# Kernel tuning notes

Hardware: AMD Instinct MI355X
Metric: run time of the kernel (lower is better)

## Reference

```python
import jax, jax.numpy as jnp
import numpy as np

B, H, W, C = 64, 56, 56, 128
NH, WS, SS = 4, 7, 3        # heads, window_size, shift_size
HID = 4 * C                  # mlp hidden
HD = C // NH                 # head dim
SCALE = HD ** -0.5
NW = (H // WS) * (W // WS)   # windows per image
L = WS * WS                  # tokens per window


def _rel_pos_index():
    coords = np.stack(np.meshgrid(np.arange(WS), np.arange(WS), indexing='ij'))  # (2,WS,WS)
    cf = coords.reshape(2, -1)
    rel = (cf[:, :, None] - cf[:, None, :]).transpose(1, 2, 0)  # (L,L,2)
    rel[:, :, 0] += WS - 1
    rel[:, :, 1] += WS - 1
    rel[:, :, 0] *= 2 * WS - 1
    return rel.sum(-1)  # (L,L) int


def _attn_mask():
    # standard Swin shifted-window mask, computed statically in numpy
    img = np.zeros((H, W), dtype=np.int32)
    cnt = 0
    for hs in (slice(0, -WS), slice(-WS, -SS), slice(-SS, None)):
        for ws_ in (slice(0, -WS), slice(-WS, -SS), slice(-SS, None)):
            img[hs, ws_] = cnt
            cnt += 1
    win = img.reshape(H // WS, WS, W // WS, WS).transpose(0, 2, 1, 3).reshape(NW, L)
    diff = win[:, None, :] - win[:, :, None]
    return np.where(diff != 0, -100.0, 0.0).astype(np.float32)  # (NW,L,L)


_REL_IDX = jnp.asarray(_rel_pos_index())
_MASK = jnp.asarray(_attn_mask())


def _layernorm(x, w, b, eps=1e-5):
    mu = x.mean(-1, keepdims=True)
    var = x.var(-1, keepdims=True)
    return (x - mu) * jax.lax.rsqrt(var + eps) * w + b


def setup_inputs() -> dict:
    key = jax.random.key(0)
    ks = jax.random.split(key, 8)
    n = lambda k, s: jax.random.normal(k, s, jnp.float32) * 0.02
    return {
        'x': jax.random.normal(ks[0], (B, H * W, C), jnp.float32),
        'norm1_w': jnp.ones((C,)), 'norm1_b': jnp.zeros((C,)),
        'qkv_w': n(ks[1], (3 * C, C)), 'qkv_b': jnp.zeros((3 * C,)),
        'proj_w': n(ks[2], (C, C)), 'proj_b': jnp.zeros((C,)),
        'rel_bias': n(ks[3], ((2 * WS - 1) ** 2, NH)),
        'norm2_w': jnp.ones((C,)), 'norm2_b': jnp.zeros((C,)),
        'fc1_w': n(ks[4], (HID, C)), 'fc1_b': jnp.zeros((HID,)),
        'fc2_w': n(ks[5], (C, HID)), 'fc2_b': jnp.zeros((C,)),
    }


def reference(x, norm1_w, norm1_b, qkv_w, qkv_b, proj_w, proj_b, rel_bias,
              norm2_w, norm2_b, fc1_w, fc1_b, fc2_w, fc2_b):
    shortcut = x
    h = _layernorm(x, norm1_w, norm1_b).reshape(B, H, W, C)
    # cyclic shift
    h = jnp.roll(h, shift=(-SS, -SS), axis=(1, 2))
    # window partition -> (B*NW, L, C)
    h = h.reshape(B, H // WS, WS, W // WS, WS, C).transpose(0, 1, 3, 2, 4, 5)
    h = h.reshape(B * NW, L, C)
    # qkv
    qkv = h @ qkv_w.T + qkv_b                      # (B*NW, L, 3C)
    qkv = qkv.reshape(B * NW, L, 3, NH, HD).transpose(2, 0, 3, 1, 4)
    q, k, v = qkv[0], qkv[1], qkv[2]               # (B*NW, NH, L, HD)
    attn = jnp.einsum('wnld,wnmd->wnlm', q * SCALE, k)  # (B*NW, NH, L, L)
    bias = rel_bias[_REL_IDX.reshape(-1)].reshape(L, L, NH).transpose(2, 0, 1)
    attn = attn + bias[None]
    # shifted-window mask
    attn = attn.reshape(B, NW, NH, L, L) + _MASK[None, :, None]
    attn = jax.nn.softmax(attn.reshape(B * NW, NH, L, L), axis=-1)
    out = jnp.einsum('wnlm,wnmd->wnld', attn, v)   # (B*NW, NH, L, HD)
    out = out.transpose(0, 2, 1, 3).reshape(B * NW, L, C)
    out = out @ proj_w.T + proj_b
    # window reverse
    out = out.reshape(B, H // WS, W // WS, WS, WS, C).transpose(0, 1, 3, 2, 4, 5)
    out = out.reshape(B, H, W, C)
    out = jnp.roll(out, shift=(SS, SS), axis=(1, 2)).reshape(B, H * W, C)
    x = shortcut + out
    # MLP
    y = _layernorm(x, norm2_w, norm2_b)
    y = jax.nn.gelu(y @ fc1_w.T + fc1_b, approximate=False)
    x = x + (y @ fc2_w.T + fc2_b)
    return x
```

## Files before the change

kernel.cpp:

```cpp
#include <hip/hip_runtime.h>
#include <math.h>


typedef unsigned int   u32;
typedef unsigned short u16;
typedef __bf16 bf16_t;
typedef __bf16 bf16x8 __attribute__((ext_vector_type(8)));
typedef float  f32x4  __attribute__((ext_vector_type(4)));

#define KSCALE 0.17677669529663687f

__device__ __forceinline__ float lo2f(u32 u){ u32 v = u << 16;         float f; __builtin_memcpy(&f,&v,4); return f; }
__device__ __forceinline__ float hi2f(u32 u){ u32 v = u & 0xffff0000u; float f; __builtin_memcpy(&f,&v,4); return f; }
__device__ __forceinline__ float b2f(u16 h){ u32 v = (u32)h << 16;     float f; __builtin_memcpy(&f,&v,4); return f; }
__device__ __forceinline__ u16  f2b(float f){ bf16_t h = (bf16_t)f; u16 u; __builtin_memcpy(&u,&h,2); return u; }
__device__ __forceinline__ u32  pack2(float a, float b){ return (u32)f2b(a) | ((u32)f2b(b) << 16); }

template<int C>
__device__ __forceinline__ float dppf(float x){
  union { float f; int i; } u; u.f = x;
  u.i = __builtin_amdgcn_update_dpp(u.i, u.i, C, 0xf, 0xf, true);
  return u.f;
}
__device__ __forceinline__ float red16max(float x){
  x = fmaxf(x, dppf<0xB1>(x));
  x = fmaxf(x, dppf<0x4E>(x));
  x = fmaxf(x, dppf<0x141>(x));
  x = fmaxf(x, dppf<0x140>(x));
  return x;
}
__device__ __forceinline__ float red16sum(float x){
  x += dppf<0xB1>(x);
  x += dppf<0x4E>(x);
  x += dppf<0x141>(x);
  x += dppf<0x140>(x);
  return x;
}
__device__ __forceinline__ float red64sum(float x){
  x = red16sum(x);
  x += __shfl_xor(x, 16, 64);
  x += __shfl_xor(x, 32, 64);
  return x;
}

template<bool F32> __device__ __forceinline__ float2 ldpair(const void* p, size_t pairIdx){
  if constexpr (F32) { return ((const float2*)p)[pairIdx]; }
  else { u32 u = ((const u32*)p)[pairIdx]; return float2{lo2f(u), hi2f(u)}; }
}
template<bool F32> __device__ __forceinline__ float ldone(const void* p, size_t i){
  if constexpr (F32) return ((const float*)p)[i];
  else               return b2f(((const u16*)p)[i]);
}
template<bool F32> __device__ __forceinline__ void stpair(void* p, size_t pairIdx, float a, float b){
  if constexpr (F32) ((float2*)p)[pairIdx] = float2{a, b};
  else               ((u32*)p)[pairIdx] = pack2(a, b);
}

__device__ __forceinline__ float gelu_f(float v){
  const float t = v * v;
  const float u = v * (1.5957691216057308f + 0.07135481282803452f * t);
  return v * __builtin_amdgcn_rcpf(1.f + __expf(-u));
}

__device__ __align__(16) u16 g_wbuf[197312];

__global__ __launch_bounds__(256) void k_cvt(const void* n1w, const void* qkvw,
    const void* projw, const void* fc1w, const void* fc2w, const void* relb)
{
  const bool bf = (((const u32*)n1w)[0] == 0x3F803F80u);
  u16* o = g_wbuf;
  if (blockIdx.x == 192) {
    const int t = threadIdx.x;
    if (t < 169) {
      const int i = t * 4;
      if (bf) { *(uint2*)(o + 196608 + i) = *(const uint2*)((const u16*)relb + i); }
      else {
        const float4 v = *(const float4*)((const float*)relb + i);
        uint2 pk; pk.x = pack2(v.x, v.y); pk.y = pack2(v.z, v.w);
        *(uint2*)(o + 196608 + i) = pk;
      }
    } else if (t < 176) {
      *(uint2*)(o + 196608 + 676 + (t - 169) * 4) = uint2{0, 0};
    }
    return;
  }
  const int i = (blockIdx.x * 256 + threadIdx.x) * 4;
  const void* src; int rel; u16* dst;
  if (i < 49152)       { src = qkvw; rel = i;          dst = o; }
  else if (i < 65536)  { src = projw; rel = i - 49152; dst = o + 49152; }
  else if (i < 131072) { src = fc1w; rel = i - 65536;  dst = o + 65536; }
  else                 { src = fc2w; rel = i - 131072; dst = o + 131072; }
  if (bf) {
    *(uint2*)(dst + rel) = *(const uint2*)((const u16*)src + rel);
  } else {
    const float4 v = *(const float4*)((const float*)src + rel);
    uint2 pk; pk.x = pack2(v.x, v.y); pk.y = pack2(v.z, v.w);
    *(uint2*)(dst + rel) = pk;
  }
}

__device__ __forceinline__ void ldBo(bf16x8 (&b)[4][2], const u16* w, int Kstr,
                                     int base, int koff, int lane)
{
  const int lr = lane & 15, quad = lane >> 4;
  const int r0 = base + 2 * lr;
  #pragma unroll
  for (int kk = 0; kk < 4; ++kk)
    #pragma unroll
    for (int nt = 0; nt < 2; ++nt)
      b[kk][nt] = *(const bf16x8*)(w + (size_t)(r0 + nt) * Kstr + koff + kk*32 + quad*8);
}
__device__ __forceinline__ void ldB(bf16x8 (&b)[4][2], const u16* w, int Kstr,
                                    int base, int lane)
{ ldBo(b, w, Kstr, base, 0, lane); }

__device__ __forceinline__ void mmB(const u16* sA, int astr, const bf16x8 (&b)[4][2],
                                    int lane, f32x4 (&acc)[4][2])
{
  const int lr = lane & 15, quad = lane >> 4;
  #pragma unroll
  for (int kk = 0; kk < 4; ++kk)
    #pragma unroll
    for (int mt = 0; mt < 4; ++mt) {
      const bf16x8 a = *(const bf16x8*)(sA + (mt*16 + lr)*astr + kk*32 + quad*8);
      acc[mt][0] = __builtin_amdgcn_mfma_f32_16x16x32_bf16(a, b[kk][0], acc[mt][0], 0, 0, 0);
      acc[mt][1] = __builtin_amdgcn_mfma_f32_16x16x32_bf16(a, b[kk][1], acc[mt][1], 0, 0, 0);
    }
}

#define A_OK  6664
#define A_OX  14112
#define A_OVT 22816
#define A_ORB 32032
#define A_SM  32712

template<bool XF32>
__device__ __forceinline__ void attn_body(
    const void* x, const void* n1w, const void* n1b,
    const void* qkvb, const void* projb, void* xout, u16* sm)
{
  u16* sQ  = sm;
  u16* sK  = sm + A_OK;
  u16* sX  = sm + A_OX;
  u16* sVt = sm + A_OVT;
  u16* sRB = sm + A_ORB;

  const int g = blockIdx.x, tid = threadIdx.x;
  const int wv = tid >> 6, lane = tid & 63, lr = lane & 15, quad = lane >> 4;
  const int b_ = g >> 6, win = g & 63, wi = win >> 3, wj = win & 7;
  const int cpi = wv * 16 + lr;

  for (int t = tid; t < 85; t += 256)
    *(uint4*)(sRB + t * 8) = *(const uint4*)(g_wbuf + 196608 + t * 8);
  if (tid < 128) {
    uint4* pz = (uint4*)(sVt + tid * 72 + 48);
    pz[0] = uint4{0,0,0,0}; pz[1] = uint4{0,0,0,0}; pz[2] = uint4{0,0,0,0};
  }
  bf16x8 b0[4][2], b1[4][2];
  ldB(b0, g_wbuf, 128, wv * 32, lane);
  const float2 w2 = ldpair<XF32>(n1w, lane), bb2 = ldpair<XF32>(n1b, lane);
  float2 xv[13];
  #pragma unroll
  for (int it = 0; it < 13; ++it) {
    const int l = wv + it * 4;
    if (l < 49) {
      const int ti = l / 7, tj = l - ti * 7;
      int si = wi * 7 + ti + 3; if (si >= 56) si -= 56;
      int sj = wj * 7 + tj + 3; if (sj >= 56) sj -= 56;
      xv[it] = ldpair<XF32>(x, ((size_t)b_ * 3136 + si * 56 + sj) * 64 + lane);
    }
  }
  #pragma unroll
  for (int it = 0; it < 13; ++it) {
    const int l = wv + it * 4;
    if (l < 49) {
      const float s = red64sum(xv[it].x + xv[it].y);
      const float q = red64sum(xv[it].x * xv[it].x + xv[it].y * xv[it].y);
      const float mean = s * (1.f / 128.f);
      const float var  = q * (1.f / 128.f) - mean * mean;
      const float rs   = rsqrtf(var + 1e-5f);
      ((u32*)sX)[l * 68 + lane] = pack2((xv[it].x - mean) * rs * w2.x + bb2.x,
                                        (xv[it].y - mean) * rs * w2.y + bb2.y);
    }
  }
  __syncthreads();

  f32x4 acc[4][2];
  #define ZACC { _Pragma("unroll") for (int mt = 0; mt < 4; ++mt) { acc[mt][0] = f32x4{0,0,0,0}; acc[mt][1] = f32x4{0,0,0,0}; } }

  ldB(b1, g_wbuf + 16384, 128, wv * 32, lane);
  ZACC; mmB(sX, 136, b0, lane, acc);
  {
    const float2 bq = ldpair<XF32>(qkvb, cpi);
    #pragma unroll
    for (int mt = 0; mt < 4; ++mt)
      #pragma unroll
      for (int rr = 0; rr < 4; ++rr) {
        const int l = mt * 16 + quad * 4 + rr;
        if (l < 49)
          ((u32*)sQ)[l * 68 + cpi] = pack2(acc[mt][0][rr] + bq.x, acc[mt][1][rr] + bq.y);
      }
  }
  ldB(b0, g_wbuf + 32768, 128, wv * 32, lane);
  ZACC; mmB(sX, 136, b1, lane, acc);
  {
    const float2 bk = ldpair<XF32>(qkvb, 64 + cpi);
    #pragma unroll
    for (int mt = 0; mt < 4; ++mt)
      #pragma unroll
      for (int rr = 0; rr < 4; ++rr) {
        const int l = mt * 16 + quad * 4 + rr;
        if (l < 49)
          ((u32*)sK)[l * 68 + cpi] = pack2(acc[mt][0][rr] + bk.x, acc[mt][1][rr] + bk.y);
      }
  }
  ldB(b1, g_wbuf + 49152, 128, wv * 32, lane);
  ZACC; mmB(sX, 136, b0, lane, acc);
  {
    const float2 bv = ldpair<XF32>(qkvb, 128 + cpi);
    const int c0 = wv * 32 + 2 * lr;
    #pragma unroll
    for (int mt = 0; mt < 4; ++mt)
      #pragma unroll
      for (int rr = 0; rr < 4; ++rr) {
        const int l = mt * 16 + quad * 4 + rr;
        if (l < 49) {
          sVt[c0 * 72 + l]       = f2b(acc[mt][0][rr] + bv.x);
          sVt[(c0 + 1) * 72 + l] = f2b(acc[mt][1][rr] + bv.y);
        }
      }
  }
  __syncthreads();

  const int hh = wv;
  f32x4 pk[4][4];
  #pragma unroll
  for (int mt = 0; mt < 4; ++mt)
    #pragma unroll
    for (int nt = 0; nt < 4; ++nt) pk[mt][nt] = f32x4{0,0,0,0};
  bf16x8 kb[4];
  #pragma unroll
  for (int nt = 0; nt < 4; ++nt)
    kb[nt] = *(const bf16x8*)(sK + (nt*16 + lr) * 136 + hh * 32 + quad * 8);
  #pragma unroll
  for (int mt = 0; mt < 4; ++mt) {
    const bf16x8 qa = *(const bf16x8*)(sQ + (mt*16 + lr) * 136 + hh * 32 + quad * 8);
    #pragma unroll
    for (int nt = 0; nt < 4; ++nt)
      pk[mt][nt] = __builtin_amdgcn_mfma_f32_16x16x32_bf16(qa, kb[nt], pk[mt][nt], 0, 0, 0);
  }

  int lcode[16], lreg[16];
  #pragma unroll
  for (int mt = 0; mt < 4; ++mt)
    #pragma unroll
    for (int rr = 0; rr < 4; ++rr) {
      const int l = mt * 16 + quad * 4 + rr;
      const int ti = l / 7, tj = l - ti * 7;
      lcode[mt*4+rr] = ti * 13 + tj;
      lreg[mt*4+rr]  = ((wi == 7) ? (ti < 4 ? 1 : 2) : 0) * 3 + ((wj == 7) ? (tj < 4 ? 1 : 2) : 0);
    }
  int mcode[4], mreg[4], mval[4];
  #pragma unroll
  for (int nt = 0; nt < 4; ++nt) {
    const int m = nt * 16 + lr;
    const int mi = m / 7, mj = m - mi * 7;
    mcode[nt] = mi * 13 + mj;
    mreg[nt]  = ((wi == 7) ? (mi < 4 ? 1 : 2) : 0) * 3 + ((wj == 7) ? (mj < 4 ? 1 : 2) : 0);
    mval[nt]  = (m < 49);
  }

  __syncthreads();

  u32 toks[16]; float2 res[16];
  #pragma unroll
  for (int mt = 0; mt < 4; ++mt)
    #pragma unroll
    for (int rr = 0; rr < 4; ++rr) {
      const int l = mt * 16 + quad * 4 + rr;
      if (l < 49) {
        const int ti = l / 7, tj = l - ti * 7;
        int si = wi * 7 + ti + 3; if (si >= 56) si -= 56;
        int sj = wj * 7 + tj + 3; if (sj >= 56) sj -= 56;
        const u32 tok = (u32)b_ * 3136 + si * 56 + sj;
        toks[mt*4+rr] = tok;
        res[mt*4+rr]  = ldpair<XF32>(x, (size_t)tok * 64 + cpi);
      }
    }

  u16* pP = sm + hh * 3528;
  float inv[16];
  #pragma unroll
  for (int i = 0; i < 16; ++i) {
    const int mt = i >> 2, rr = i & 3;
    const int l = mt * 16 + quad * 4 + rr;
    float v[4];
    #pragma unroll
    for (int nt = 0; nt < 4; ++nt) {
      float t = pk[mt][nt][rr] * KSCALE + b2f(sRB[(lcode[i] - mcode[nt] + 84) * 4 + hh]);
      if (lreg[i] != mreg[nt]) t -= 100.f;
      if (!mval[nt]) t = -1e30f;
      v[nt] = t;
    }
    const float mx = red16max(fmaxf(fmaxf(v[0], v[1]), fmaxf(v[2], v[3])));
    float e[4];
    float s = 0.f;
    #pragma unroll
    for (int nt = 0; nt < 4; ++nt) { e[nt] = __expf(v[nt] - mx); s += e[nt]; }
    s = red16sum(s);
    inv[i] = __builtin_amdgcn_rcpf(s);
    if (l < 49) {
      #pragma unroll
      for (int nt = 0; nt < 4; ++nt) pP[l * 72 + nt * 16 + lr] = f2b(e[nt]);
    }
  }
  asm volatile("s_waitcnt lgkmcnt(0)" ::: "memory");

  f32x4 ov[4][2];
  #pragma unroll
  for (int mt = 0; mt < 4; ++mt) { ov[mt][0] = f32x4{0,0,0,0}; ov[mt][1] = f32x4{0,0,0,0}; }
  #pragma unroll
  for (int k2 = 0; k2 < 2; ++k2) {
    bf16x8 vb[2];
    #pragma unroll
    for (int nd = 0; nd < 2; ++nd)
      vb[nd] = *(const bf16x8*)(sVt + (hh * 32 + 2 * lr + nd) * 72 + k2 * 32 + quad * 8);
    #pragma unroll
    for (int mt = 0; mt < 4; ++mt) {
      const bf16x8 pa = *(const bf16x8*)(pP + (mt * 16 + lr) * 72 + k2 * 32 + quad * 8);
      #pragma unroll
      for (int nd = 0; nd < 2; ++nd)
        ov[mt][nd] = __builtin_amdgcn_mfma_f32_16x16x32_bf16(pa, vb[nd], ov[mt][nd], 0, 0, 0);
    }
  }
  #pragma unroll
  for (int i = 0; i < 16; ++i) {
    const int mt = i >> 2, rr = i & 3;
    const int l = mt * 16 + quad * 4 + rr;
    if (l < 49)
      ((u32*)sX)[l * 68 + hh * 16 + lr] = pack2(ov[mt][0][rr] * inv[i], ov[mt][1][rr] * inv[i]);
  }
  __syncthreads();

  const float2 pb = ldpair<XF32>(projb, cpi);
  ZACC; mmB(sX, 136, b1, lane, acc);
  #pragma unroll
  for (int mt = 0; mt < 4; ++mt)
    #pragma unroll
    for (int rr = 0; rr < 4; ++rr) {
      const int l = mt * 16 + quad * 4 + rr;
      if (l < 49)
        stpair<XF32>(xout, (size_t)toks[mt*4+rr] * 64 + cpi,
                     acc[mt][0][rr] + pb.x + res[mt*4+rr].x,
                     acc[mt][1][rr] + pb.y + res[mt*4+rr].y);
    }
  #undef ZACC
}

__global__ __launch_bounds__(256, 2) void k_attn(
    const void* x, const void* n1w, const void* n1b,
    const void* qkvb, const void* projb, void* xout)
{
  __shared__ __align__(16) u16 sm[A_SM];
  if (((const u32*)n1w)[0] == 0x3F803F80u)
    attn_body<false>(x, n1w, n1b, qkvb, projb, xout, sm);
  else
    attn_body<true >(x, n1w, n1b, qkvb, projb, xout, sm);
}

template<bool XF32>
__device__ __forceinline__ void mlp_body(
    void* xio, const void* n2w, const void* n2b,
    const void* fc1b, const void* fc2b, u16* sXN, u16* sH)
{
  const int blkm = blockIdx.x, tid = threadIdx.x;
  const int wv = tid >> 6, lane = tid & 63, lr = lane & 15, quad = lane >> 4;
  const int cpi = wv * 16 + lr;

  const float2 w2 = ldpair<XF32>(n2w, lane), bb2 = ldpair<XF32>(n2b, lane);
  float2 xv[16];
  #pragma unroll
  for (int it = 0; it < 16; ++it)
    xv[it] = ldpair<XF32>(xio, ((size_t)blkm * 64 + wv + it * 4) * 64 + lane);
  #pragma unroll
  for (int it = 0; it < 16; ++it) {
    const int r = wv + it * 4;
    const float s = red64sum(xv[it].x + xv[it].y);
    const float q = red64sum(xv[it].x * xv[it].x + xv[it].y * xv[it].y);
    const float mean = s * (1.f / 128.f);
    const float var  = q * (1.f / 128.f) - mean * mean;
    const float rs   = rsqrtf(var + 1e-5f);
    ((u32*)sXN)[r * 68 + lane] = pack2((xv[it].x - mean) * rs * w2.x + bb2.x,
                                       (xv[it].y - mean) * rs * w2.y + bb2.y);
  }
  __syncthreads();

  f32x4 acc2[4][2];
  #pragma unroll
  for (int mt = 0; mt < 4; ++mt) { acc2[mt][0] = f32x4{0,0,0,0}; acc2[mt][1] = f32x4{0,0,0,0}; }
  float2 rp[16];

  bf16x8 f1e[4][2], f1o[4][2], f2[4][2];
  ldB(f1e, g_wbuf + 65536, 128, wv * 32, lane);
  #pragma unroll
  for (int ch = 0; ch < 4; ++ch) {
    if (ch) __syncthreads();
    ldBo(f2, g_wbuf + 131072, 512, wv * 32, ch * 128, lane);
    if (ch < 3) {
      if (ch & 1) ldB(f1e, g_wbuf + 65536, 128, (ch + 1) * 128 + wv * 32, lane);
      else        ldB(f1o, g_wbuf + 65536, 128, (ch + 1) * 128 + wv * 32, lane);
    }
    const bf16x8 (&curB)[4][2] = (ch & 1) ? f1o : f1e;
    f32x4 a1[4][2];
    #pragma unroll
    for (int mt = 0; mt < 4; ++mt) { a1[mt][0] = f32x4{0,0,0,0}; a1[mt][1] = f32x4{0,0,0,0}; }
    mmB(sXN, 136, curB, lane, a1);
    const float2 gb = ldpair<XF32>(fc1b, ch * 64 + cpi);
    #pragma unroll
    for (int mt = 0; mt < 4; ++mt)
      #pragma unroll
      for (int rr = 0; rr < 4; ++rr) {
        const int l = mt * 16 + quad * 4 + rr;
        ((u32*)sH)[l * 68 + cpi] = pack2(gelu_f(a1[mt][0][rr] + gb.x),
                                         gelu_f(a1[mt][1][rr] + gb.y));
      }
    if (ch == 3) {
      #pragma unroll
      for (int mt = 0; mt < 4; ++mt)
        #pragma unroll
        for (int rr = 0; rr < 4; ++rr) {
          const size_t m = (size_t)blkm * 64 + mt * 16 + quad * 4 + rr;
          rp[mt*4+rr] = ldpair<XF32>(xio, m * 64 + cpi);
        }
    }
    __syncthreads();
    mmB(sH, 136, f2, lane, acc2);
  }

  const float2 fb = ldpair<XF32>(fc2b, cpi);
  #pragma unroll
  for (int mt = 0; mt < 4; ++mt)
    #pragma unroll
    for (int rr = 0; rr < 4; ++rr) {
      const size_t m = (size_t)blkm * 64 + mt * 16 + quad * 4 + rr;
      stpair<XF32>(xio, m * 64 + cpi,
                   acc2[mt][0][rr] + fb.x + rp[mt*4+rr].x,
                   acc2[mt][1][rr] + fb.y + rp[mt*4+rr].y);
    }
}

__global__ __launch_bounds__(256, 4) void k_mlp(
    void* xio, const void* n2w, const void* n2b,
    const void* fc1b, const void* fc2b)
{
  __shared__ __align__(16) u16 sXN[64 * 136];
  __shared__ __align__(16) u16 sH[64 * 136];
  if (((const u32*)n2w)[0] == 0x3F803F80u)
    mlp_body<false>(xio, n2w, n2b, fc1b, fc2b, sXN, sH);
  else
    mlp_body<true >(xio, n2w, n2b, fc1b, fc2b, sXN, sH);
}

extern "C" void kernel_launch(void* const* d_in, const int* in_sizes, int n_in,
                              void* d_out, int out_size, void* d_ws, size_t ws_size,
                              hipStream_t stream) {
  k_cvt<<<dim3(193), dim3(256), 0, stream>>>(
      d_in[1], d_in[3], d_in[5], d_in[10], d_in[12], d_in[7]);
  k_attn<<<dim3(4096), dim3(256), 0, stream>>>(
      d_in[0], d_in[1], d_in[2], d_in[4], d_in[6], d_out);
  k_mlp <<<dim3(3136), dim3(256), 0, stream>>>(
      d_out, d_in[8], d_in[9], d_in[11], d_in[13]);
}
```

Before: 406.8 us.

## Fuse window attention and MLP into one kernel per window

Merges the attention kernel and the MLP kernel into a single kernel where each block processes one window. The post-attention residual is kept in shared memory as fp32 and fed straight into LayerNorm2 and the MLP, so the intermediate never makes a global round trip and one launch goes away. In exchange, shared memory per block grows, and the MLP now runs on 49-token tiles padded to 64 rows instead of dense 64-row tiles, which wastes some MFMA work. Occupancy is also limited by the attention kernel's launch bounds.

After: 421.9 us. 3.7% more time.

```diff
diff --git a/kernel.cpp b/kernel.cpp
--- a/kernel.cpp
+++ b/kernel.cpp
@@ -46,10 +46,6 @@
 template<bool F32> __device__ __forceinline__ float2 ldpair(const void* p, size_t pairIdx){
   if constexpr (F32) { return ((const float2*)p)[pairIdx]; }
   else { u32 u = ((const u32*)p)[pairIdx]; return float2{lo2f(u), hi2f(u)}; }
-}
-template<bool F32> __device__ __forceinline__ float ldone(const void* p, size_t i){
-  if constexpr (F32) return ((const float*)p)[i];
-  else               return b2f(((const u16*)p)[i]);
 }
 template<bool F32> __device__ __forceinline__ void stpair(void* p, size_t pairIdx, float a, float b){
   if constexpr (F32) ((float2*)p)[pairIdx] = float2{a, b};
@@ -128,16 +124,19 @@
     }
 }
 
-#define A_OK  6664
-#define A_OX  14112
-#define A_OVT 22816
-#define A_ORB 32032
-#define A_SM  32712
+#define A_OK   6664
+#define A_OX   14112
+#define A_OVT  22816
+#define A_OX2  22816
+#define A_ORB  39456
+#define A_SM   40136
 
 template<bool XF32>
-__device__ __forceinline__ void attn_body(
+__device__ __forceinline__ void fused_body(
     const void* x, const void* n1w, const void* n1b,
-    const void* qkvb, const void* projb, void* xout, u16* sm)
+    const void* qkvb, const void* projb,
+    const void* n2w, const void* n2b,
+    const void* fc1b, const void* fc2b, void* xout, u16* sm)
 {
   u16* sQ  = sm;
   u16* sK  = sm + A_OK;
@@ -342,66 +341,48 @@
   }
   __syncthreads();
 
+  float* pX2 = (float*)(sm + A_OX2);
   const float2 pb = ldpair<XF32>(projb, cpi);
+  bf16x8 f1e[4][2], f1o[4][2];
   ZACC; mmB(sX, 136, b1, lane, acc);
+  ldB(f1e, g_wbuf + 65536, 128, wv * 32, lane);
   #pragma unroll
   for (int mt = 0; mt < 4; ++mt)
     #pragma unroll
     for (int rr = 0; rr < 4; ++rr) {
       const int l = mt * 16 + quad * 4 + rr;
       if (l < 49)
-        stpair<XF32>(xout, (size_t)toks[mt*4+rr] * 64 + cpi,
-                     acc[mt][0][rr] + pb.x + res[mt*4+rr].x,
-                     acc[mt][1][rr] + pb.y + res[mt*4+rr].y);
-    }
-  #undef ZACC
-}
-
-__global__ __launch_bounds__(256, 2) void k_attn(
-    const void* x, const void* n1w, const void* n1b,
-    const void* qkvb, const void* projb, void* xout)
-{
-  __shared__ __align__(16) u16 sm[A_SM];
-  if (((const u32*)n1w)[0] == 0x3F803F80u)
-    attn_body<false>(x, n1w, n1b, qkvb, projb, xout, sm);
-  else
-    attn_body<true >(x, n1w, n1b, qkvb, projb, xout, sm);
-}
-
-template<bool XF32>
-__device__ __forceinline__ void mlp_body(
-    void* xio, const void* n2w, const void* n2b,
-    const void* fc1b, const void* fc2b, u16* sXN, u16* sH)
-{
-  const int blkm = blockIdx.x, tid = threadIdx.x;
-  const int wv = tid >> 6, lane = tid & 63, lr = lane & 15, quad = lane >> 4;
-  const int cpi = wv * 16 + lr;
-
-  const float2 w2 = ldpair<XF32>(n2w, lane), bb2 = ldpair<XF32>(n2b, lane);
-  float2 xv[16];
-  #pragma unroll
-  for (int it = 0; it < 16; ++it)
-    xv[it] = ldpair<XF32>(xio, ((size_t)blkm * 64 + wv + it * 4) * 64 + lane);
-  #pragma unroll
-  for (int it = 0; it < 16; ++it) {
-    const int r = wv + it * 4;
-    const float s = red64sum(xv[it].x + xv[it].y);
-    const float q = red64sum(xv[it].x * xv[it].x + xv[it].y * xv[it].y);
-    const float mean = s * (1.f / 128.f);
-    const float var  = q * (1.f / 128.f) - mean * mean;
-    const float rs   = rsqrtf(var + 1e-5f);
-    ((u32*)sXN)[r * 68 + lane] = pack2((xv[it].x - mean) * rs * w2.x + bb2.x,
-                                       (xv[it].y - mean) * rs * w2.y + bb2.y);
+        *(float2*)(pX2 + l * 130 + 2 * cpi) =
+            float2{acc[mt][0][rr] + pb.x + res[mt*4+rr].x,
+                   acc[mt][1][rr] + pb.y + res[mt*4+rr].y};
+    }
+  __syncthreads();
+
+  u16* sXN = sX;
+  u16* sH  = sm;
+  {
+    const float2 m2w = ldpair<XF32>(n2w, lane), m2b = ldpair<XF32>(n2b, lane);
+    #pragma unroll
+    for (int it = 0; it < 13; ++it) {
+      const int l = wv + it * 4;
+      if (l < 49) {
+        const float2 x2 = *(const float2*)(pX2 + l * 130 + 2 * lane);
+        const float s = red64sum(x2.x + x2.y);
+        const float q = red64sum(x2.x * x2.x + x2.y * x2.y);
+        const float mean = s * (1.f / 128.f);
+        const float var  = q * (1.f / 128.f) - mean * mean;
+        const float rs   = rsqrtf(var + 1e-5f);
+        ((u32*)sXN)[l * 68 + lane] = pack2((x2.x - mean) * rs * m2w.x + m2b.x,
+                                           (x2.y - mean) * rs * m2w.y + m2b.y);
+      }
+    }
   }
   __syncthreads();
 
   f32x4 acc2[4][2];
   #pragma unroll
   for (int mt = 0; mt < 4; ++mt) { acc2[mt][0] = f32x4{0,0,0,0}; acc2[mt][1] = f32x4{0,0,0,0}; }
-  float2 rp[16];
-
-  bf16x8 f1e[4][2], f1o[4][2], f2[4][2];
-  ldB(f1e, g_wbuf + 65536, 128, wv * 32, lane);
+  bf16x8 f2[4][2];
   #pragma unroll
   for (int ch = 0; ch < 4; ++ch) {
     if (ch) __syncthreads();
@@ -424,15 +405,6 @@
         ((u32*)sH)[l * 68 + cpi] = pack2(gelu_f(a1[mt][0][rr] + gb.x),
                                          gelu_f(a1[mt][1][rr] + gb.y));
       }
-    if (ch == 3) {
-      #pragma unroll
-      for (int mt = 0; mt < 4; ++mt)
-        #pragma unroll
-        for (int rr = 0; rr < 4; ++rr) {
-          const size_t m = (size_t)blkm * 64 + mt * 16 + quad * 4 + rr;
-          rp[mt*4+rr] = ldpair<XF32>(xio, m * 64 + cpi);
-        }
-    }
     __syncthreads();
     mmB(sH, 136, f2, lane, acc2);
   }
@@ -442,23 +414,28 @@
   for (int mt = 0; mt < 4; ++mt)
     #pragma unroll
     for (int rr = 0; rr < 4; ++rr) {
-      const size_t m = (size_t)blkm * 64 + mt * 16 + quad * 4 + rr;
-      stpair<XF32>(xio, m * 64 + cpi,
-                   acc2[mt][0][rr] + fb.x + rp[mt*4+rr].x,
-                   acc2[mt][1][rr] + fb.y + rp[mt*4+rr].y);
-    }
-}
-
-__global__ __launch_bounds__(256, 4) void k_mlp(
-    void* xio, const void* n2w, const void* n2b,
-    const void* fc1b, const void* fc2b)
+      const int l = mt * 16 + quad * 4 + rr;
+      if (l < 49) {
+        const float2 x2 = *(const float2*)(pX2 + l * 130 + 2 * cpi);
+        stpair<XF32>(xout, (size_t)toks[mt*4+rr] * 64 + cpi,
+                     acc2[mt][0][rr] + fb.x + x2.x,
+                     acc2[mt][1][rr] + fb.y + x2.y);
+      }
+    }
+  #undef ZACC
+}
+
+__global__ __launch_bounds__(256, 2) void k_fused(
+    const void* x, const void* n1w, const void* n1b,
+    const void* qkvb, const void* projb,
+    const void* n2w, const void* n2b,
+    const void* fc1b, const void* fc2b, void* xout)
 {
-  __shared__ __align__(16) u16 sXN[64 * 136];
-  __shared__ __align__(16) u16 sH[64 * 136];
-  if (((const u32*)n2w)[0] == 0x3F803F80u)
-    mlp_body<false>(xio, n2w, n2b, fc1b, fc2b, sXN, sH);
+  __shared__ __align__(16) u16 sm[A_SM];
+  if (((const u32*)n1w)[0] == 0x3F803F80u)
+    fused_body<false>(x, n1w, n1b, qkvb, projb, n2w, n2b, fc1b, fc2b, xout, sm);
   else
-    mlp_body<true >(xio, n2w, n2b, fc1b, fc2b, sXN, sH);
+    fused_body<true >(x, n1w, n1b, qkvb, projb, n2w, n2b, fc1b, fc2b, xout, sm);
 }
 
 extern "C" void kernel_launch(void* const* d_in, const int* in_sizes, int n_in,
@@ -466,8 +443,7 @@
                               hipStream_t stream) {
   k_cvt<<<dim3(193), dim3(256), 0, stream>>>(
       d_in[1], d_in[3], d_in[5], d_in[10], d_in[12], d_in[7]);
-  k_attn<<<dim3(4096), dim3(256), 0, stream>>>(
-      d_in[0], d_in[1], d_in[2], d_in[4], d_in[6], d_out);
-  k_mlp <<<dim3(3136), dim3(256), 0, stream>>>(
-      d_out, d_in[8], d_in[9], d_in[11], d_in[13]);
-}
+  k_fused<<<dim3(4096), dim3(256), 0, stream>>>(
+      d_in[0], d_in[1], d_in[2], d_in[4], d_in[6],
+      d_in[8], d_in[9], d_in[11], d_in[13], d_out);
+}
```

## Split MLP hidden dimension into smaller chunks to cut registers and LDS

Applied to the files above, without the earlier changes.

The MLP kernel now walks the 512-wide hidden dimension in eight chunks of 64 instead of four chunks of 128. Each wave computes one 16-column slab of fc1 per chunk and accumulates a 64-deep slice into fc2. This shrinks the hidden staging buffer in LDS, drops the double-buffered fc1 weight registers and moves the residual reload to the end. The aim is to lower register and LDS pressure so launch bounds can rise from 4 to 6 blocks per CU. In exchange there are twice as many barriers, smaller MFMA batches per sync, and less prefetch overlap of weight loads.

New measurement: 404.6 us. About the same (-0.5%).

```diff
diff --git a/kernel.cpp b/kernel.cpp
--- a/kernel.cpp
+++ b/kernel.cpp
@@ -128,6 +128,19 @@
     }
 }
 
+__device__ __forceinline__ void mmB16(const u16* sA, int astr, const bf16x8 (&b)[4],
+                                      int lane, f32x4 (&acc)[4])
+{
+  const int lr = lane & 15, quad = lane >> 4;
+  #pragma unroll
+  for (int kk = 0; kk < 4; ++kk)
+    #pragma unroll
+    for (int mt = 0; mt < 4; ++mt) {
+      const bf16x8 a = *(const bf16x8*)(sA + (mt*16 + lr)*astr + kk*32 + quad*8);
+      acc[mt] = __builtin_amdgcn_mfma_f32_16x16x32_bf16(a, b[kk], acc[mt], 0, 0, 0);
+    }
+}
+
 #define A_OK  6664
 #define A_OX  14112
 #define A_OVT 22816
@@ -378,66 +391,80 @@
   const int cpi = wv * 16 + lr;
 
   const float2 w2 = ldpair<XF32>(n2w, lane), bb2 = ldpair<XF32>(n2b, lane);
-  float2 xv[16];
-  #pragma unroll
-  for (int it = 0; it < 16; ++it)
-    xv[it] = ldpair<XF32>(xio, ((size_t)blkm * 64 + wv + it * 4) * 64 + lane);
-  #pragma unroll
-  for (int it = 0; it < 16; ++it) {
-    const int r = wv + it * 4;
-    const float s = red64sum(xv[it].x + xv[it].y);
-    const float q = red64sum(xv[it].x * xv[it].x + xv[it].y * xv[it].y);
-    const float mean = s * (1.f / 128.f);
-    const float var  = q * (1.f / 128.f) - mean * mean;
-    const float rs   = rsqrtf(var + 1e-5f);
-    ((u32*)sXN)[r * 68 + lane] = pack2((xv[it].x - mean) * rs * w2.x + bb2.x,
-                                       (xv[it].y - mean) * rs * w2.y + bb2.y);
+  {
+    float2 xv[16];
+    #pragma unroll
+    for (int it = 0; it < 16; ++it)
+      xv[it] = ldpair<XF32>(xio, ((size_t)blkm * 64 + wv + it * 4) * 64 + lane);
+    #pragma unroll
+    for (int it = 0; it < 16; ++it) {
+      const int r = wv + it * 4;
+      const float s = red64sum(xv[it].x + xv[it].y);
+      const float q = red64sum(xv[it].x * xv[it].x + xv[it].y * xv[it].y);
+      const float mean = s * (1.f / 128.f);
+      const float var  = q * (1.f / 128.f) - mean * mean;
+      const float rs   = rsqrtf(var + 1e-5f);
+      ((u32*)sXN)[r * 68 + lane] = pack2((xv[it].x - mean) * rs * w2.x + bb2.x,
+                                         (xv[it].y - mean) * rs * w2.y + bb2.y);
+    }
   }
   __syncthreads();
 
   f32x4 acc2[4][2];
   #pragma unroll
   for (int mt = 0; mt < 4; ++mt) { acc2[mt][0] = f32x4{0,0,0,0}; acc2[mt][1] = f32x4{0,0,0,0}; }
-  float2 rp[16];
-
-  bf16x8 f1e[4][2], f1o[4][2], f2[4][2];
-  ldB(f1e, g_wbuf + 65536, 128, wv * 32, lane);
-  #pragma unroll
-  for (int ch = 0; ch < 4; ++ch) {
+
+  for (int ch = 0; ch < 8; ++ch) {
     if (ch) __syncthreads();
-    ldBo(f2, g_wbuf + 131072, 512, wv * 32, ch * 128, lane);
-    if (ch < 3) {
-      if (ch & 1) ldB(f1e, g_wbuf + 65536, 128, (ch + 1) * 128 + wv * 32, lane);
-      else        ldB(f1o, g_wbuf + 65536, 128, (ch + 1) * 128 + wv * 32, lane);
-    }
-    const bf16x8 (&curB)[4][2] = (ch & 1) ? f1o : f1e;
-    f32x4 a1[4][2];
-    #pragma unroll
-    for (int mt = 0; mt < 4; ++mt) { a1[mt][0] = f32x4{0,0,0,0}; a1[mt][1] = f32x4{0,0,0,0}; }
-    mmB(sXN, 136, curB, lane, a1);
-    const float2 gb = ldpair<XF32>(fc1b, ch * 64 + cpi);
+
+    const int hc = ch * 64 + cpi;
+    bf16x8 f1[4];
+    #pragma unroll
+    for (int kk = 0; kk < 4; ++kk)
+      f1[kk] = *(const bf16x8*)(g_wbuf + 65536 + (size_t)hc * 128 + kk*32 + quad*8);
+    f32x4 a1[4];
+    #pragma unroll
+    for (int mt = 0; mt < 4; ++mt) a1[mt] = f32x4{0,0,0,0};
+    mmB16(sXN, 136, f1, lane, a1);
+
+    const float gb = ldone<XF32>(fc1b, hc);
     #pragma unroll
     for (int mt = 0; mt < 4; ++mt)
       #pragma unroll
       for (int rr = 0; rr < 4; ++rr) {
         const int l = mt * 16 + quad * 4 + rr;
-        ((u32*)sH)[l * 68 + cpi] = pack2(gelu_f(a1[mt][0][rr] + gb.x),
-                                         gelu_f(a1[mt][1][rr] + gb.y));
-      }
-    if (ch == 3) {
-      #pragma unroll
-      for (int mt = 0; mt < 4; ++mt)
-        #pragma unroll
-        for (int rr = 0; rr < 4; ++rr) {
-          const size_t m = (size_t)blkm * 64 + mt * 16 + quad * 4 + rr;
-          rp[mt*4+rr] = ldpair<XF32>(xio, m * 64 + cpi);
-        }
-    }
+        sH[l * 72 + cpi] = f2b(gelu_f(a1[mt][rr] + gb));
+      }
+
+    bf16x8 f2[2][2];
+    #pragma unroll
+    for (int kk = 0; kk < 2; ++kk)
+      #pragma unroll
+      for (int nt = 0; nt < 2; ++nt)
+        f2[kk][nt] = *(const bf16x8*)(g_wbuf + 131072 +
+                        (size_t)(2*cpi + nt) * 512 + ch*64 + kk*32 + quad*8);
+
     __syncthreads();
-    mmB(sH, 136, f2, lane, acc2);
+
+    #pragma unroll
+    for (int kk = 0; kk < 2; ++kk)
+      #pragma unroll
+      for (int mt = 0; mt < 4; ++mt) {
+        const bf16x8 a = *(const bf16x8*)(sH + (mt*16 + lr)*72 + kk*32 + quad*8);
+        acc2[mt][0] = __builtin_amdgcn_mfma_f32_16x16x32_bf16(a, f2[kk][0], acc2[mt][0], 0, 0, 0);
+        acc2[mt][1] = __builtin_amdgcn_mfma_f32_16x16x32_bf16(a, f2[kk][1], acc2[mt][1], 0, 0, 0);
+      }
   }
 
   const float2 fb = ldpair<XF32>(fc2b, cpi);
+  float2 rp[16];
+  #pragma unroll
+  for (int mt = 0; mt < 4; ++mt)
+    #pragma unroll
+    for (int rr = 0; rr < 4; ++rr) {
+      const size_t m = (size_t)blkm * 64 + mt * 16 + quad * 4 + rr;
+      rp[mt*4+rr] = ldpair<XF32>(xio, m * 64 + cpi);
+    }
   #pragma unroll
   for (int mt = 0; mt < 4; ++mt)
     #pragma unroll
@@ -449,12 +476,12 @@
     }
 }
 
-__global__ __launch_bounds__(256, 4) void k_mlp(
+__global__ __launch_bounds__(256, 6) void k_mlp(
     void* xio, const void* n2w, const void* n2b,
     const void* fc1b, const void* fc2b)
 {
   __shared__ __align__(16) u16 sXN[64 * 136];
-  __shared__ __align__(16) u16 sH[64 * 136];
+  __shared__ __align__(16) u16 sH[64 * 72];
   if (((const u32*)n2w)[0] == 0x3F803F80u)
     mlp_body<false>(xio, n2w, n2b, fc1b, fc2b, sXN, sH);
   else
```
